# Optimization experiments

Measured on AMD Instinct MI355X. Metric: run time of the kernel, lower is better.

The kernel has to match this reference:

```python
import jax, jax.numpy as jnp
import numpy as np

MARGIN = 500.0


def setup_inputs() -> dict:
    key = jax.random.key(0)
    k1, k2 = jax.random.split(key)
    N, D = 32768, 3
    batched_labels = jax.random.randint(k1, (N,), 0, 100, dtype=jnp.int64 if jax.config.jax_enable_x64 else jnp.int32).astype(jnp.int32)
    batched_predicted_coords = jax.random.normal(k2, (N, D), dtype=jnp.float32)
    return {"batched_labels": batched_labels, "batched_predicted_coords": batched_predicted_coords}


def reference(batched_labels, batched_predicted_coords):
    # Faithful to the original: the Python loop overwrites `loss` each
    # iteration, so only the LAST anchor (i = N-1) contributes.
    anchor_lab = batched_labels[-1]
    anchor_pt = batched_predicted_coords[-1]  # [D]
    # labels: 0 if same label as anchor, 1 otherwise
    lab = jnp.where(batched_labels == anchor_lab, 0.0, 1.0)  # [N]
    diff = anchor_pt[None, :] - batched_predicted_coords  # [N, D]
    dist = jnp.sum(diff * diff, axis=1)  # squared euclidean distance, [N]
    loss = (1.0 - lab) * dist + lab * jnp.maximum(0.0, MARGIN - dist)
    return loss.sum()
```

## Files before the change

### kernel.cpp

```cpp
#include <hip/hip_runtime.h>

#define MARGIN 500.0f

__global__ __launch_bounds__(256) void custom_loss_kernel(
        const int* __restrict__ labels,
        const float* __restrict__ coords,
        float* __restrict__ out, int N) {
    const int   anchor_lab = labels[N - 1];
    const float ax = coords[3 * (N - 1) + 0];
    const float ay = coords[3 * (N - 1) + 1];
    const float az = coords[3 * (N - 1) + 2];

    const int i = blockIdx.x * blockDim.x + threadIdx.x;
    float v = 0.0f;
    if (i < N) {
        const float dx = ax - coords[3 * i + 0];
        const float dy = ay - coords[3 * i + 1];
        const float dz = az - coords[3 * i + 2];
        const float dist = dx * dx + dy * dy + dz * dz;
        v = (labels[i] == anchor_lab) ? dist : fmaxf(0.0f, MARGIN - dist);
    }

    #pragma unroll
    for (int off = 32; off > 0; off >>= 1)
        v += __shfl_down(v, off, 64);

    __shared__ float smem[4];
    const int wave = threadIdx.x >> 6;
    const int lane = threadIdx.x & 63;
    if (lane == 0) smem[wave] = v;
    __syncthreads();

    if (threadIdx.x == 0) {
        const float s = smem[0] + smem[1] + smem[2] + smem[3];
        atomicAdd(out, s);
    }
}

extern "C" void kernel_launch(void* const* d_in, const int* in_sizes, int n_in,
                              void* d_out, int out_size, void* d_ws, size_t ws_size,
                              hipStream_t stream) {
    const int*   labels = (const int*)d_in[0];
    const float* coords = (const float*)d_in[1];
    float*       out    = (float*)d_out;
    const int N = in_sizes[0];

    hipMemsetAsync(out, 0, sizeof(float), stream);

    const int block = 256;
    const int grid  = (N + block - 1) / block;
    custom_loss_kernel<<<grid, block, 0, stream>>>(labels, coords, out, N);
}
```

Before: 57.50 us.

## Use single-block kernel with vectorized loads, drop memset and atomics

Replaces the multi-block grid plus memset and atomicAdd with one 1024-thread block that loops over groups of four points using float4 and int4 loads, then writes the result directly. This removes the extra memset launch and the atomic contention and widens the loads. The trade-off is that all 393 KB of input is read by a single CU, which limits bandwidth. The code also silently drops the tail when N is not a multiple of 4.

```diff
diff --git a/kernel.cpp b/kernel.cpp
--- a/kernel.cpp
+++ b/kernel.cpp
@@ -2,38 +2,64 @@
 
 #define MARGIN 500.0f
 
-__global__ __launch_bounds__(256) void custom_loss_kernel(
+__global__ __launch_bounds__(1024) void custom_loss_onepass(
         const int* __restrict__ labels,
         const float* __restrict__ coords,
         float* __restrict__ out, int N) {
+    const int t = threadIdx.x;
+
     const int   anchor_lab = labels[N - 1];
     const float ax = coords[3 * (N - 1) + 0];
     const float ay = coords[3 * (N - 1) + 1];
     const float az = coords[3 * (N - 1) + 2];
 
-    const int i = blockIdx.x * blockDim.x + threadIdx.x;
+    const float4* __restrict__ c4 = (const float4*)coords;
+    const int4*   __restrict__ l4 = (const int4*)labels;
+
+    const int ngroups = N >> 2;
     float v = 0.0f;
-    if (i < N) {
-        const float dx = ax - coords[3 * i + 0];
-        const float dy = ay - coords[3 * i + 1];
-        const float dz = az - coords[3 * i + 2];
-        const float dist = dx * dx + dy * dy + dz * dz;
-        v = (labels[i] == anchor_lab) ? dist : fmaxf(0.0f, MARGIN - dist);
+    for (int g = t; g < ngroups; g += 1024) {
+        const float4 p0 = c4[3 * g + 0];
+        const float4 p1 = c4[3 * g + 1];
+        const float4 p2 = c4[3 * g + 2];
+        const int4   lb = l4[g];
+        {
+            const float dx = ax - p0.x, dy = ay - p0.y, dz = az - p0.z;
+            const float d = dx * dx + dy * dy + dz * dz;
+            v += (lb.x == anchor_lab) ? d : fmaxf(0.0f, MARGIN - d);
+        }
+        {
+            const float dx = ax - p0.w, dy = ay - p1.x, dz = az - p1.y;
+            const float d = dx * dx + dy * dy + dz * dz;
+            v += (lb.y == anchor_lab) ? d : fmaxf(0.0f, MARGIN - d);
+        }
+        {
+            const float dx = ax - p1.z, dy = ay - p1.w, dz = az - p2.x;
+            const float d = dx * dx + dy * dy + dz * dz;
+            v += (lb.z == anchor_lab) ? d : fmaxf(0.0f, MARGIN - d);
+        }
+        {
+            const float dx = ax - p2.y, dy = ay - p2.z, dz = az - p2.w;
+            const float d = dx * dx + dy * dy + dz * dz;
+            v += (lb.w == anchor_lab) ? d : fmaxf(0.0f, MARGIN - d);
+        }
     }
 
     #pragma unroll
     for (int off = 32; off > 0; off >>= 1)
         v += __shfl_down(v, off, 64);
 
-    __shared__ float smem[4];
-    const int wave = threadIdx.x >> 6;
-    const int lane = threadIdx.x & 63;
+    __shared__ float smem[16];
+    const int wave = t >> 6;
+    const int lane = t & 63;
     if (lane == 0) smem[wave] = v;
     __syncthreads();
 
-    if (threadIdx.x == 0) {
-        const float s = smem[0] + smem[1] + smem[2] + smem[3];
-        atomicAdd(out, s);
+    if (t == 0) {
+        float s = 0.0f;
+        #pragma unroll
+        for (int i = 0; i < 16; ++i) s += smem[i];
+        out[0] = s;
     }
 }
 
@@ -45,9 +71,5 @@
     float*       out    = (float*)d_out;
     const int N = in_sizes[0];
 
-    hipMemsetAsync(out, 0, sizeof(float), stream);
-
-    const int block = 256;
-    const int grid  = (N + block - 1) / block;
-    custom_loss_kernel<<<grid, block, 0, stream>>>(labels, coords, out, N);
+    custom_loss_onepass<<<1, 1024, 0, stream>>>(labels, coords, out, N);
 }
```

Result: slower. 59.57 us (+3.6%).
